# Kernel optimization log

Hardware: AMD Instinct MI355X
Metric: run time of the kernel (lower is better)

## Reference

```python
import jax, jax.numpy as jnp
import numpy as np

B = 32768          # number of trees
DEPTH = 3          # perfect binary trees: 8 leaves each
N_LEAF = B * (1 << DEPTH)
V, X, H, C = 32000, 256, 128, 5


def _apply_iou(iou, c, b_iou):
    # iou: [n, 3H], c: [n, H]
    i, o, u = jnp.split(iou + b_iou, 3, axis=1)
    c = jax.nn.sigmoid(i) * jnp.tanh(u) + c
    h = jax.nn.sigmoid(o) * jnp.tanh(c)
    return h, c


def setup_inputs() -> dict:
    key = jax.random.key(0)
    ks = jax.random.split(key, 8)
    rng = np.random.default_rng(0)

    # per-level random node orderings -> irregular child gathers
    sizes = [N_LEAF >> l for l in range(DEPTH + 1)]  # [8B, 4B, 2B, B]
    perms = [rng.permutation(s).astype(np.int32) for s in sizes]
    parts = []
    for l in range(1, DEPTH + 1):
        n = sizes[l]
        k = np.arange(n)
        ci = np.empty((n, 2), np.int32)
        # canonical node k at level l has children 2k, 2k+1 at level l-1
        ci[perms[l]] = np.stack([perms[l - 1][2 * k], perms[l - 1][2 * k + 1]], 1)
        parts.append(ci)
    child_idx = jnp.asarray(np.concatenate(parts, 0))  # [4B+2B+B, 2]

    leaf_x = jax.random.randint(ks[0], (N_LEAF,), 0, V, dtype=jnp.int32)
    sc = 0.02
    return {
        "leaf_x": leaf_x,
        "child_idx": child_idx,
        "emb": jax.random.normal(ks[1], (V, X), jnp.float32) * sc,
        "W_iou": jax.random.normal(ks[2], (3 * H, X), jnp.float32) * sc,
        "U_iou": jax.random.normal(ks[3], (3 * H, 2 * H), jnp.float32) * sc,
        "b_iou": jnp.zeros((3 * H,), jnp.float32),
        "U_f": jax.random.normal(ks[4], (2 * H, 2 * H), jnp.float32) * sc,
        "b_f": jnp.zeros((2 * H,), jnp.float32),
        "W_lin": jax.random.normal(ks[5], (C, H), jnp.float32) * sc,
        "b_lin": jnp.zeros((C,), jnp.float32),
    }


def reference(leaf_x, child_idx, emb, W_iou, U_iou, b_iou, U_f, b_f, W_lin, b_lin):
    # Leaves: embedding -> W_iou -> gates with c=0 (dropout is identity in eval)
    embeds = emb[leaf_x]                       # [N_leaf, X]
    iou = embeds @ W_iou.T                     # [N_leaf, 3H]
    h, c = _apply_iou(iou, jnp.zeros((leaf_x.shape[0], H), iou.dtype), b_iou)

    hs = [h]
    n, offset, total = leaf_x.shape[0], 0, child_idx.shape[0]
    while offset < total:  # one iteration per tree level (static)
        n //= 2
        ci = child_idx[offset:offset + n]       # [n, 2] -> prev-level rows
        offset += n
        h_ch = h[ci]                            # [n, 2, H] irregular gather
        c_ch = c[ci]                            # [n, 2, H]
        h_cat = h_ch.reshape(n, 2 * H)
        f = jax.nn.sigmoid(h_cat @ U_f.T + b_f).reshape(n, 2, H)
        c_sum = jnp.sum(f * c_ch, axis=1)       # [n, H]
        iou = h_cat @ U_iou.T                   # [n, 3H]
        h, c = _apply_iou(iou, c_sum, b_iou)
        hs.append(h)

    h_all = jnp.concatenate(hs, axis=0)         # [N_total, H]
    logits = h_all @ W_lin.T + b_lin            # [N_total, C]
    return logits
```

## Files before the change

### kernel.cpp

```cpp
#include <hip/hip_runtime.h>
#include <hip/hip_bf16.h>
#include <stdint.h>


#define THREADS 512

typedef __attribute__((ext_vector_type(8))) short short8;
typedef __attribute__((ext_vector_type(4))) float f32x4;

__device__ __forceinline__ unsigned short f2bf(float x) {
    unsigned u = __float_as_uint(x);
    u += 0x7fffu + ((u >> 16) & 1u);
    return (unsigned short)(u >> 16);
}
__device__ __forceinline__ float bf2f(unsigned short b) {
    return __uint_as_float(((unsigned)b) << 16);
}
__device__ __forceinline__ float rcp_fast(float x) { return __builtin_amdgcn_rcpf(x); }
__device__ __forceinline__ float sigm(float x) { return rcp_fast(1.f + __expf(-x)); }
__device__ __forceinline__ float tanh_fast(float x) {
    float e = __expf(2.f * x);
    return (e - 1.f) * rcp_fast(e + 1.f);
}

__global__ __launch_bounds__(256)
void prep_kernel(const float* __restrict__ W_iou,
                 const float* __restrict__ U_iou,
                 const float* __restrict__ U_f,
                 unsigned short* __restrict__ Wl,
                 unsigned short* __restrict__ Wc)
{
    const int i = blockIdx.x * 256 + threadIdx.x;
    if (i < 98304) {
        Wl[i] = f2bf(W_iou[i]);
        Wc[i] = f2bf(U_iou[i]);
    }
    if (i < 65536) {
        Wc[98304 + i] = f2bf(U_f[i]);
    }
}

template<int NCOL, int G, int CW, bool WC>
__device__ __forceinline__ void level_step(
    const unsigned short* __restrict__ Wg,
    const unsigned char* Blds,
    unsigned char* h_out,
    unsigned short* cAr,
    const float* __restrict__ b_iou, const float* __restrict__ b_f,
    int w, int lrow, int lk, int slotBase, int mrows)
{
    const int q0 = w * 16;
    const unsigned char* wbase = reinterpret_cast<const unsigned char*>(Wg)
                               + (q0 + lrow) * 512 + lk * 16;

    f32x4 acc[NCOL][G];
    #pragma unroll
    for (int j = 0; j < NCOL; ++j)
        #pragma unroll
        for (int g = 0; g < G; ++g)
            acc[j][g] = (f32x4){0.f, 0.f, 0.f, 0.f};

    #pragma unroll
    for (int ks = 0; ks < 8; ++ks) {
        short8 aW[NCOL];
        #pragma unroll
        for (int j = 0; j < NCOL; ++j)
            aW[j] = *reinterpret_cast<const short8*>(
                wbase + j * 65536 + ks * 64);
        #pragma unroll
        for (int g = 0; g < G; ++g) {
            const int row = g * 16 + lrow;
            const int chunk = (ks * 4 + lk) ^ (row & 7);
            short8 bN = *reinterpret_cast<const short8*>(
                Blds + row * 512 + (chunk << 4));
            #pragma unroll
            for (int j = 0; j < NCOL; ++j)
                acc[j][g] = __builtin_amdgcn_mfma_f32_16x16x32_bf16(
                    aW[j], bN, acc[j][g], 0, 0, 0);
        }
    }

    #pragma unroll
    for (int g = 0; g < G; ++g) {
        const int mlB = g * 16 + lrow;
        if (mlB < mrows) {
            const int ml = slotBase + mlB;
            #pragma unroll
            for (int r = 0; r < 4; ++r) {
                const int p = q0 + lk * 4 + r;
                float iv = acc[0][g][r] + b_iou[p];
                float ov = acc[1][g][r] + b_iou[128 + p];
                float uv = acc[2][g][r] + b_iou[256 + p];
                float csum = 0.f;
                if (NCOL == 5) {
                    float f0 = acc[3][g][r] + b_f[p];
                    float f1 = acc[4][g][r] + b_f[128 + p];
                    const int cb = p * 66 + CW * mlB;
                    csum = sigm(f0) * bf2f(cAr[cb])
                         + sigm(f1) * bf2f(cAr[cb + CW / 2]);
                }
                float cv = sigm(iv) * tanh_fast(uv) + csum;
                float hv = sigm(ov) * tanh_fast(cv);
                if (WC) cAr[p * 66 + CW * ml] = f2bf(cv);
                const int jr = ml >> 1;
                const int q = (ml & 1) * 16 + (p >> 3);
                *reinterpret_cast<unsigned short*>(
                    h_out + jr * 512 + ((q ^ (jr & 7)) << 4) + (p & 7) * 2)
                    = f2bf(hv);
            }
        }
    }
}

__device__ __forceinline__ void logits_emit(
    const unsigned char* h_lds, int M, const int* idsLds, int idBase,
    int segOff, const float* __restrict__ W_lin, const float* __restrict__ b_lin,
    float* __restrict__ out, int t)
{
    const int s = t >> 2, sub = t & 3;
    if (s >= M) return;
    float hv[32];
    const int j = s >> 1;
    #pragma unroll
    for (int qq = 0; qq < 4; ++qq) {
        const int q = (s & 1) * 16 + sub * 4 + qq;
        short8 v = *reinterpret_cast<const short8*>(
            h_lds + j * 512 + ((q ^ (j & 7)) << 4));
        #pragma unroll
        for (int e = 0; e < 8; ++e) hv[qq * 8 + e] = bf2f((unsigned short)v[e]);
    }
    const int gid = idsLds ? idsLds[s] : (idBase + s);
    float dots[5];
    #pragma unroll
    for (int cl = 0; cl < 5; ++cl) {
        const float* wr = W_lin + cl * 128 + sub * 32;
        float d = 0.f;
        #pragma unroll
        for (int k = 0; k < 32; ++k) d += hv[k] * wr[k];
        d += __shfl_xor(d, 1);
        d += __shfl_xor(d, 2);
        dots[cl] = d;
    }
    if (sub == 0) {
        float* op = out + (size_t)(segOff + gid) * 5;
        #pragma unroll
        for (int cl = 0; cl < 5; ++cl)
            op[cl] = dots[cl] + b_lin[cl];
    }
}

__global__ __launch_bounds__(THREADS, 4)
void tree_kernel(const int*  __restrict__ leaf_x,
                 const int2* __restrict__ cpairs,
                 const float* __restrict__ emb,
                 const unsigned short* __restrict__ Wl,
                 const unsigned short* __restrict__ Wc,
                 const float* __restrict__ b_iou,
                 const float* __restrict__ b_f,
                 const float* __restrict__ W_lin,
                 const float* __restrict__ b_lin,
                 float* __restrict__ out)
{
    __shared__ __align__(16) unsigned char arena[49664];
    __shared__ int ids0[64], ids1[32], ids2[16], tok[64];

    const int t    = threadIdx.x;
    const int lane = t & 63;
    const int w    = t >> 6;
    const int lrow = lane & 15;
    const int lk   = lane >> 4;
    const int blk3 = blockIdx.x * 8;

    if (t < 8)  { int2 p = cpairs[196608 + blk3 + t]; ids2[2*t] = p.x; ids2[2*t+1] = p.y; }
    __syncthreads();
    if (t < 16) { int2 p = cpairs[131072 + ids2[t]];  ids1[2*t] = p.x; ids1[2*t+1] = p.y; }
    __syncthreads();
    if (t < 32) { int2 p = cpairs[ids1[t]];           ids0[2*t] = p.x; ids0[2*t+1] = p.y; }
    __syncthreads();
    if (t < 64) { tok[t] = leaf_x[ids0[t]]; }
    __syncthreads();

    unsigned char*  X0  = arena;
    unsigned char*  h0  = arena + 16384;
    unsigned short* cAr = (unsigned short*)(arena + 32768);
    unsigned char*  h1  = arena;
    unsigned char*  h2  = arena + 16384;
    unsigned char*  h3  = arena + 8192;

    #pragma unroll 1
    for (int half = 0; half < 2; ++half) {
        {
            const int c  = t & 31;
            const int r0 = t >> 5;
            #pragma unroll
            for (int rr = 0; rr < 2; ++rr) {
                const int r  = r0 + rr * 16;
                const int gi = tok[half * 32 + r];
                const float4* src = reinterpret_cast<const float4*>(
                    emb + (size_t)gi * 256 + c * 8);
                float4 a = src[0], b = src[1];
                short8 v;
                v[0]=(short)f2bf(a.x); v[1]=(short)f2bf(a.y);
                v[2]=(short)f2bf(a.z); v[3]=(short)f2bf(a.w);
                v[4]=(short)f2bf(b.x); v[5]=(short)f2bf(b.y);
                v[6]=(short)f2bf(b.z); v[7]=(short)f2bf(b.w);
                *reinterpret_cast<short8*>(X0 + r * 512 + ((c ^ (r & 7)) << 4)) = v;
            }
        }
        __syncthreads();
        level_step<3, 2, 1, true>(Wl, X0, h0, cAr, b_iou, b_f,
                                  w, lrow, lk, half * 32, 32);
        __syncthreads();
    }

    logits_emit(h0, 64, ids0, 0, 0, W_lin, b_lin, out, t);
    level_step<5, 2, 2, true>(Wc, h0, h1, cAr, b_iou, b_f,
                              w, lrow, lk, 0, 32);
    __syncthreads();

    logits_emit(h1, 32, ids1, 0, 262144, W_lin, b_lin, out, t);
    level_step<5, 1, 4, true>(Wc, h1, h2, cAr, b_iou, b_f,
                              w, lrow, lk, 0, 16);
    __syncthreads();

    logits_emit(h2, 16, ids2, 0, 393216, W_lin, b_lin, out, t);
    level_step<5, 1, 8, false>(Wc, h2, h3, cAr, b_iou, b_f,
                               w, lrow, lk, 0, 8);
    __syncthreads();

    logits_emit(h3, 8, nullptr, blk3, 458752, W_lin, b_lin, out, t);
}

extern "C" void kernel_launch(void* const* d_in, const int* in_sizes, int n_in,
                              void* d_out, int out_size, void* d_ws, size_t ws_size,
                              hipStream_t stream)
{
    const int*   leaf_x = (const int*)d_in[0];
    const int*   child  = (const int*)d_in[1];
    const float* emb    = (const float*)d_in[2];
    const float* W_iou  = (const float*)d_in[3];
    const float* U_iou  = (const float*)d_in[4];
    const float* b_iou  = (const float*)d_in[5];
    const float* U_f    = (const float*)d_in[6];
    const float* b_f    = (const float*)d_in[7];
    const float* W_lin  = (const float*)d_in[8];
    const float* b_lin  = (const float*)d_in[9];
    float* out = (float*)d_out;

    char* ws = (char*)d_ws;
    unsigned short* Wl = (unsigned short*)ws;
    unsigned short* Wc = (unsigned short*)(ws + 196608);

    prep_kernel<<<384, 256, 0, stream>>>(W_iou, U_iou, U_f, Wl, Wc);

    tree_kernel<<<4096, THREADS, 0, stream>>>(
        leaf_x, (const int2*)child, emb, Wl, Wc,
        b_iou, b_f, W_lin, b_lin, out);
}
```

Baseline: 903.4 us.

## Stage logits densely per block and scatter in a separate kernel; cache biases in LDS

Instead of each block writing its 5-float logits directly to scattered output rows, the tree kernel now stores its 120 logit rows densely in workspace together with an index map, and a new scatter kernel writes them to their final positions and adds b_lin. The iou/f biases and W_lin are also copied into shared memory once per block, which removes repeated global loads in the gate epilogue and the logit dot products. The logit computation is restructured to accumulate straight from LDS weights. The cost is an extra kernel launch, an extra round trip of about 10 MB through workspace, and more LDS per block, which could lower occupancy.

```diff
diff --git a/kernel.cpp b/kernel.cpp
--- a/kernel.cpp
+++ b/kernel.cpp
@@ -46,7 +46,7 @@
     const unsigned char* Blds,
     unsigned char* h_out,
     unsigned short* cAr,
-    const float* __restrict__ b_iou, const float* __restrict__ b_f,
+    const float* bias,
     int w, int lrow, int lk, int slotBase, int mrows)
 {
     const int q0 = w * 16;
@@ -88,13 +88,13 @@
             #pragma unroll
             for (int r = 0; r < 4; ++r) {
                 const int p = q0 + lk * 4 + r;
-                float iv = acc[0][g][r] + b_iou[p];
-                float ov = acc[1][g][r] + b_iou[128 + p];
-                float uv = acc[2][g][r] + b_iou[256 + p];
+                float iv = acc[0][g][r] + bias[p];
+                float ov = acc[1][g][r] + bias[128 + p];
+                float uv = acc[2][g][r] + bias[256 + p];
                 float csum = 0.f;
                 if (NCOL == 5) {
-                    float f0 = acc[3][g][r] + b_f[p];
-                    float f1 = acc[4][g][r] + b_f[128 + p];
+                    float f0 = acc[3][g][r] + bias[384 + p];
+                    float f1 = acc[4][g][r] + bias[512 + p];
                     const int cb = p * 66 + CW * mlB;
                     csum = sigm(f0) * bf2f(cAr[cb])
                          + sigm(f1) * bf2f(cAr[cb + CW / 2]);
@@ -112,41 +112,49 @@
     }
 }
 
-__device__ __forceinline__ void logits_emit(
-    const unsigned char* h_lds, int M, const int* idsLds, int idBase,
-    int segOff, const float* __restrict__ W_lin, const float* __restrict__ b_lin,
-    float* __restrict__ out, int t)
+__device__ __forceinline__ void logits_stash(
+    const unsigned char* h_lds, int M, int stBase,
+    const float* Wl_lds, float* sL, int t)
 {
     const int s = t >> 2, sub = t & 3;
     if (s >= M) return;
-    float hv[32];
     const int j = s >> 1;
+    float dots[5] = {0.f, 0.f, 0.f, 0.f, 0.f};
     #pragma unroll
     for (int qq = 0; qq < 4; ++qq) {
         const int q = (s & 1) * 16 + sub * 4 + qq;
         short8 v = *reinterpret_cast<const short8*>(
             h_lds + j * 512 + ((q ^ (j & 7)) << 4));
         #pragma unroll
-        for (int e = 0; e < 8; ++e) hv[qq * 8 + e] = bf2f((unsigned short)v[e]);
-    }
-    const int gid = idsLds ? idsLds[s] : (idBase + s);
-    float dots[5];
+        for (int e = 0; e < 8; ++e) {
+            const float hv = bf2f((unsigned short)v[e]);
+            const int k = sub * 32 + qq * 8 + e;
+            #pragma unroll
+            for (int cl = 0; cl < 5; ++cl)
+                dots[cl] += hv * Wl_lds[cl * 128 + k];
+        }
+    }
     #pragma unroll
     for (int cl = 0; cl < 5; ++cl) {
-        const float* wr = W_lin + cl * 128 + sub * 32;
-        float d = 0.f;
-        #pragma unroll
-        for (int k = 0; k < 32; ++k) d += hv[k] * wr[k];
+        float d = dots[cl];
         d += __shfl_xor(d, 1);
         d += __shfl_xor(d, 2);
-        dots[cl] = d;
-    }
-    if (sub == 0) {
-        float* op = out + (size_t)(segOff + gid) * 5;
-        #pragma unroll
-        for (int cl = 0; cl < 5; ++cl)
-            op[cl] = dots[cl] + b_lin[cl];
-    }
+        if (sub == 0) sL[(stBase + s) * 5 + cl] = d;
+    }
+}
+
+__global__ __launch_bounds__(256)
+void scatter_kernel(const float* __restrict__ dense,
+                    const int* __restrict__ map,
+                    const float* __restrict__ b_lin,
+                    float* __restrict__ out)
+{
+    const int i = blockIdx.x * 256 + threadIdx.x;
+    const int g = map[i];
+    const float* sp = dense + (size_t)i * 5;
+    float* op = out + (size_t)g * 5;
+    #pragma unroll
+    for (int c = 0; c < 5; ++c) op[c] = sp[c] + b_lin[c];
 }
 
 __global__ __launch_bounds__(THREADS, 4)
@@ -158,11 +166,13 @@
                  const float* __restrict__ b_iou,
                  const float* __restrict__ b_f,
                  const float* __restrict__ W_lin,
-                 const float* __restrict__ b_lin,
-                 float* __restrict__ out)
+                 float* __restrict__ denseL,
+                 int* __restrict__ mapL)
 {
     __shared__ __align__(16) unsigned char arena[49664];
-    __shared__ int ids0[64], ids1[32], ids2[16], tok[64];
+    __shared__ int ids0[64], ids1[32], ids2[16], tok[64], sg[120];
+    __shared__ float sL[600];
+    __shared__ float bias[1280];
 
     const int t    = threadIdx.x;
     const int lane = t & 63;
@@ -171,13 +181,25 @@
     const int lk   = lane >> 4;
     const int blk3 = blockIdx.x * 8;
 
+    #pragma unroll
+    for (int i = t; i < 1280; i += THREADS) {
+        float v;
+        if (i < 384)      v = b_iou[i];
+        else if (i < 640) v = b_f[i - 384];
+        else              v = W_lin[i - 640];
+        bias[i] = v;
+    }
+
     if (t < 8)  { int2 p = cpairs[196608 + blk3 + t]; ids2[2*t] = p.x; ids2[2*t+1] = p.y; }
     __syncthreads();
     if (t < 16) { int2 p = cpairs[131072 + ids2[t]];  ids1[2*t] = p.x; ids1[2*t+1] = p.y; }
     __syncthreads();
     if (t < 32) { int2 p = cpairs[ids1[t]];           ids0[2*t] = p.x; ids0[2*t+1] = p.y; }
     __syncthreads();
-    if (t < 64) { tok[t] = leaf_x[ids0[t]]; }
+    if      (t < 64)  { tok[t] = leaf_x[ids0[t]]; sg[t] = ids0[t]; }
+    else if (t < 96)  { sg[t] = 262144 + ids1[t - 64]; }
+    else if (t < 112) { sg[t] = 393216 + ids2[t - 96]; }
+    else if (t < 120) { sg[t] = 458752 + blk3 + (t - 112); }
     __syncthreads();
 
     unsigned char*  X0  = arena;
@@ -186,6 +208,7 @@
     unsigned char*  h1  = arena;
     unsigned char*  h2  = arena + 16384;
     unsigned char*  h3  = arena + 8192;
+    const float*    WlL = bias + 640;
 
     #pragma unroll 1
     for (int half = 0; half < 2; ++half) {
@@ -208,27 +231,35 @@
             }
         }
         __syncthreads();
-        level_step<3, 2, 1, true>(Wl, X0, h0, cAr, b_iou, b_f,
+        level_step<3, 2, 1, true>(Wl, X0, h0, cAr, bias,
                                   w, lrow, lk, half * 32, 32);
         __syncthreads();
     }
 
-    logits_emit(h0, 64, ids0, 0, 0, W_lin, b_lin, out, t);
-    level_step<5, 2, 2, true>(Wc, h0, h1, cAr, b_iou, b_f,
+    logits_stash(h0, 64, 0, WlL, sL, t);
+    level_step<5, 2, 2, true>(Wc, h0, h1, cAr, bias,
                               w, lrow, lk, 0, 32);
     __syncthreads();
 
-    logits_emit(h1, 32, ids1, 0, 262144, W_lin, b_lin, out, t);
-    level_step<5, 1, 4, true>(Wc, h1, h2, cAr, b_iou, b_f,
+    logits_stash(h1, 32, 64, WlL, sL, t);
+    level_step<5, 1, 4, true>(Wc, h1, h2, cAr, bias,
                               w, lrow, lk, 0, 16);
     __syncthreads();
 
-    logits_emit(h2, 16, ids2, 0, 393216, W_lin, b_lin, out, t);
-    level_step<5, 1, 8, false>(Wc, h2, h3, cAr, b_iou, b_f,
+    logits_stash(h2, 16, 96, WlL, sL, t);
+    level_step<5, 1, 8, false>(Wc, h2, h3, cAr, bias,
                                w, lrow, lk, 0, 8);
     __syncthreads();
 
-    logits_emit(h3, 8, nullptr, blk3, 458752, W_lin, b_lin, out, t);
+    logits_stash(h3, 8, 112, WlL, sL, t);
+    __syncthreads();
+
+    {
+        float* dL = denseL + (size_t)blockIdx.x * 600;
+        int*   mp = mapL   + (size_t)blockIdx.x * 120;
+        if (t < 120) mp[t] = sg[t];
+        for (int i = t; i < 600; i += THREADS) dL[i] = sL[i];
+    }
 }
 
 extern "C" void kernel_launch(void* const* d_in, const int* in_sizes, int n_in,
@@ -250,10 +281,14 @@
     char* ws = (char*)d_ws;
     unsigned short* Wl = (unsigned short*)ws;
     unsigned short* Wc = (unsigned short*)(ws + 196608);
+    float* denseL = (float*)(ws + 524288);
+    int*   mapL   = (int*)(ws + 524288 + 9830400);
 
     prep_kernel<<<384, 256, 0, stream>>>(W_iou, U_iou, U_f, Wl, Wc);
 
     tree_kernel<<<4096, THREADS, 0, stream>>>(
         leaf_x, (const int2*)child, emb, Wl, Wc,
-        b_iou, b_f, W_lin, b_lin, out);
-}
+        b_iou, b_f, W_lin, denseL, mapL);
+
+    scatter_kernel<<<1920, 256, 0, stream>>>(denseL, mapL, b_lin, out);
+}
```

New measurement: 928.2 us. +2.7%, slower.

## Split tree kernel into per-level wave kernels with global h/c buffers

Applied to the files above, without the earlier changes.

Replaces the single block-per-8-trees kernel with a multi-launch pipeline. Child-index chasing kernels first build per-level node id lists. Then one wave-per-16-nodes MFMA kernel runs per level, storing h and c in workspace in bf16, with logits fused into the epilogue. This removes the LDS-heavy, sync-bound fused design and its low-occupancy 512-thread blocks, but adds global round trips for h/c, extra launches, and per-wave weight reloads from L2. The old fused kernel is kept as a fallback when the workspace is too small.

```diff
diff --git a/kernel.cpp b/kernel.cpp
--- a/kernel.cpp
+++ b/kernel.cpp
@@ -2,8 +2,6 @@
 #include <hip/hip_bf16.h>
 #include <stdint.h>
 
-
-#define THREADS 512
 
 typedef __attribute__((ext_vector_type(8))) short short8;
 typedef __attribute__((ext_vector_type(4))) float f32x4;
@@ -40,33 +38,174 @@
     }
 }
 
+__global__ __launch_bounds__(256)
+void chase_kernel(const int2* __restrict__ cp, const int* __restrict__ src,
+                  int srcBase, int n, int* __restrict__ dst)
+{
+    const int i = blockIdx.x * 256 + threadIdx.x;
+    if (i < n) {
+        const int s = src ? src[i] : srcBase + i;
+        const int2 c = cp[s];
+        dst[2 * i]     = c.x;
+        dst[2 * i + 1] = c.y;
+    }
+}
+
+template<int NCOL, bool LEAF, bool STORE_HC>
+__global__ __launch_bounds__(256)
+void wave_level(const unsigned short* __restrict__ Wg,
+                const int*  __restrict__ idlist,
+                int idbase,
+                const int*  __restrict__ leafx,
+                const float* __restrict__ emb,
+                const unsigned short* __restrict__ hprev,
+                const unsigned short* __restrict__ cprev,
+                unsigned short* __restrict__ hout,
+                unsigned short* __restrict__ cout,
+                const float* __restrict__ b_iou,
+                const float* __restrict__ b_f,
+                const float* __restrict__ W_lin,
+                const float* __restrict__ b_lin,
+                float* __restrict__ out, int segOff, int nnodes)
+{
+    const int lane = threadIdx.x & 63;
+    const int nb   = (blockIdx.x * 4 + (threadIdx.x >> 6)) * 16;
+    if (nb >= nnodes) return;
+    const int lrow = lane & 15;
+    const int lk   = lane >> 4;
+
+    short8 aN[8];
+    if (LEAF) {
+        const int li = idlist ? idlist[nb + lrow] : idbase + nb + lrow;
+        const int gi = leafx[li];
+        const float* er = emb + (size_t)gi * 256;
+        #pragma unroll
+        for (int ks = 0; ks < 8; ++ks) {
+            const float4 a = *reinterpret_cast<const float4*>(er + ks * 32 + lk * 8);
+            const float4 b = *reinterpret_cast<const float4*>(er + ks * 32 + lk * 8 + 4);
+            short8 v;
+            v[0]=(short)f2bf(a.x); v[1]=(short)f2bf(a.y);
+            v[2]=(short)f2bf(a.z); v[3]=(short)f2bf(a.w);
+            v[4]=(short)f2bf(b.x); v[5]=(short)f2bf(b.y);
+            v[6]=(short)f2bf(b.z); v[7]=(short)f2bf(b.w);
+            aN[ks] = v;
+        }
+    } else {
+        #pragma unroll
+        for (int ks = 0; ks < 8; ++ks) {
+            const int child = 2 * (nb + lrow) + (ks >= 4 ? 1 : 0);
+            aN[ks] = *reinterpret_cast<const short8*>(
+                hprev + (size_t)child * 128 + (ks & 3) * 32 + lk * 8);
+        }
+    }
+
+    int gidr[4];
+    #pragma unroll
+    for (int r = 0; r < 4; ++r) {
+        const int i = nb + lk * 4 + r;
+        gidr[r] = idlist ? idlist[i] : idbase + i;
+    }
+
+    float lgt[5][4];
+    #pragma unroll
+    for (int cl = 0; cl < 5; ++cl)
+        #pragma unroll
+        for (int r = 0; r < 4; ++r) lgt[cl][r] = 0.f;
+
+    for (int pb = 0; pb < 128; pb += 16) {
+        f32x4 acc[NCOL];
+        #pragma unroll
+        for (int j = 0; j < NCOL; ++j) acc[j] = (f32x4){0.f, 0.f, 0.f, 0.f};
+
+        #pragma unroll
+        for (int ks = 0; ks < 8; ++ks) {
+            short8 bW[NCOL];
+            #pragma unroll
+            for (int j = 0; j < NCOL; ++j)
+                bW[j] = *reinterpret_cast<const short8*>(
+                    Wg + (size_t)(j * 128 + pb + lrow) * 256 + ks * 32 + lk * 8);
+            #pragma unroll
+            for (int j = 0; j < NCOL; ++j)
+                acc[j] = __builtin_amdgcn_mfma_f32_16x16x32_bf16(
+                    aN[ks], bW[j], acc[j], 0, 0, 0);
+        }
+
+        const int p = pb + lrow;
+        const float bi = b_iou[p], bo = b_iou[128 + p], bu = b_iou[256 + p];
+        float bf0 = 0.f, bf1 = 0.f;
+        if (NCOL == 5) { bf0 = b_f[p]; bf1 = b_f[128 + p]; }
+        float wl[5];
+        #pragma unroll
+        for (int cl = 0; cl < 5; ++cl) wl[cl] = W_lin[cl * 128 + p];
+
+        #pragma unroll
+        for (int r = 0; r < 4; ++r) {
+            const int i = nb + lk * 4 + r;
+            const float iv = acc[0][r] + bi;
+            const float ov = acc[1][r] + bo;
+            const float uv = acc[2][r] + bu;
+            float csum = 0.f;
+            if (NCOL == 5) {
+                const float c0 = bf2f(cprev[(size_t)(2 * i) * 128 + p]);
+                const float c1 = bf2f(cprev[(size_t)(2 * i + 1) * 128 + p]);
+                csum = sigm(acc[3][r] + bf0) * c0 + sigm(acc[4][r] + bf1) * c1;
+            }
+            const float cv = sigm(iv) * tanh_fast(uv) + csum;
+            const float hv = sigm(ov) * tanh_fast(cv);
+            if (STORE_HC) {
+                hout[(size_t)i * 128 + p] = f2bf(hv);
+                cout[(size_t)i * 128 + p] = f2bf(cv);
+            }
+            #pragma unroll
+            for (int cl = 0; cl < 5; ++cl) lgt[cl][r] += hv * wl[cl];
+        }
+    }
+
+    #pragma unroll
+    for (int cl = 0; cl < 5; ++cl)
+        #pragma unroll
+        for (int r = 0; r < 4; ++r) {
+            float d = lgt[cl][r];
+            d += __shfl_xor(d, 1);
+            d += __shfl_xor(d, 2);
+            d += __shfl_xor(d, 4);
+            d += __shfl_xor(d, 8);
+            lgt[cl][r] = d;
+        }
+    if (lrow < 5) {
+        const float bl = b_lin[lrow];
+        #pragma unroll
+        for (int r = 0; r < 4; ++r) {
+            float v = (lrow == 0) ? lgt[0][r] : (lrow == 1) ? lgt[1][r]
+                    : (lrow == 2) ? lgt[2][r] : (lrow == 3) ? lgt[3][r] : lgt[4][r];
+            out[(size_t)(segOff + gidr[r]) * 5 + lrow] = v + bl;
+        }
+    }
+}
+
+#define FB_THREADS 512
+
 template<int NCOL, int G, int CW, bool WC>
-__device__ __forceinline__ void level_step(
+__device__ __forceinline__ void fb_level_step(
     const unsigned short* __restrict__ Wg,
-    const unsigned char* Blds,
-    unsigned char* h_out,
-    unsigned short* cAr,
+    const unsigned char* Blds, unsigned char* h_out, unsigned short* cAr,
     const float* __restrict__ b_iou, const float* __restrict__ b_f,
     int w, int lrow, int lk, int slotBase, int mrows)
 {
     const int q0 = w * 16;
     const unsigned char* wbase = reinterpret_cast<const unsigned char*>(Wg)
                                + (q0 + lrow) * 512 + lk * 16;
-
     f32x4 acc[NCOL][G];
     #pragma unroll
     for (int j = 0; j < NCOL; ++j)
         #pragma unroll
-        for (int g = 0; g < G; ++g)
-            acc[j][g] = (f32x4){0.f, 0.f, 0.f, 0.f};
-
+        for (int g = 0; g < G; ++g) acc[j][g] = (f32x4){0.f, 0.f, 0.f, 0.f};
     #pragma unroll
     for (int ks = 0; ks < 8; ++ks) {
         short8 aW[NCOL];
         #pragma unroll
         for (int j = 0; j < NCOL; ++j)
-            aW[j] = *reinterpret_cast<const short8*>(
-                wbase + j * 65536 + ks * 64);
+            aW[j] = *reinterpret_cast<const short8*>(wbase + j * 65536 + ks * 64);
         #pragma unroll
         for (int g = 0; g < G; ++g) {
             const int row = g * 16 + lrow;
@@ -79,7 +218,6 @@
                     aW[j], bN, acc[j][g], 0, 0, 0);
         }
     }
-
     #pragma unroll
     for (int g = 0; g < G; ++g) {
         const int mlB = g * 16 + lrow;
@@ -96,8 +234,7 @@
                     float f0 = acc[3][g][r] + b_f[p];
                     float f1 = acc[4][g][r] + b_f[128 + p];
                     const int cb = p * 66 + CW * mlB;
-                    csum = sigm(f0) * bf2f(cAr[cb])
-                         + sigm(f1) * bf2f(cAr[cb + CW / 2]);
+                    csum = sigm(f0) * bf2f(cAr[cb]) + sigm(f1) * bf2f(cAr[cb + CW / 2]);
                 }
                 float cv = sigm(iv) * tanh_fast(uv) + csum;
                 float hv = sigm(ov) * tanh_fast(cv);
@@ -105,14 +242,13 @@
                 const int jr = ml >> 1;
                 const int q = (ml & 1) * 16 + (p >> 3);
                 *reinterpret_cast<unsigned short*>(
-                    h_out + jr * 512 + ((q ^ (jr & 7)) << 4) + (p & 7) * 2)
-                    = f2bf(hv);
+                    h_out + jr * 512 + ((q ^ (jr & 7)) << 4) + (p & 7) * 2) = f2bf(hv);
             }
         }
     }
 }
 
-__device__ __forceinline__ void logits_emit(
+__device__ __forceinline__ void fb_logits_emit(
     const unsigned char* h_lds, int M, const int* idsLds, int idBase,
     int segOff, const float* __restrict__ W_lin, const float* __restrict__ b_lin,
     float* __restrict__ out, int t)
@@ -144,33 +280,27 @@
     if (sub == 0) {
         float* op = out + (size_t)(segOff + gid) * 5;
         #pragma unroll
-        for (int cl = 0; cl < 5; ++cl)
-            op[cl] = dots[cl] + b_lin[cl];
-    }
-}
-
-__global__ __launch_bounds__(THREADS, 4)
-void tree_kernel(const int*  __restrict__ leaf_x,
-                 const int2* __restrict__ cpairs,
-                 const float* __restrict__ emb,
-                 const unsigned short* __restrict__ Wl,
-                 const unsigned short* __restrict__ Wc,
-                 const float* __restrict__ b_iou,
-                 const float* __restrict__ b_f,
-                 const float* __restrict__ W_lin,
-                 const float* __restrict__ b_lin,
-                 float* __restrict__ out)
+        for (int cl = 0; cl < 5; ++cl) op[cl] = dots[cl] + b_lin[cl];
+    }
+}
+
+__global__ __launch_bounds__(FB_THREADS, 4)
+void fb_tree_kernel(const int*  __restrict__ leaf_x,
+                    const int2* __restrict__ cpairs,
+                    const float* __restrict__ emb,
+                    const unsigned short* __restrict__ Wl,
+                    const unsigned short* __restrict__ Wc,
+                    const float* __restrict__ b_iou,
+                    const float* __restrict__ b_f,
+                    const float* __restrict__ W_lin,
+                    const float* __restrict__ b_lin,
+                    float* __restrict__ out)
 {
     __shared__ __align__(16) unsigned char arena[49664];
     __shared__ int ids0[64], ids1[32], ids2[16], tok[64];
-
-    const int t    = threadIdx.x;
-    const int lane = t & 63;
-    const int w    = t >> 6;
-    const int lrow = lane & 15;
-    const int lk   = lane >> 4;
+    const int t = threadIdx.x, lane = t & 63, w = t >> 6;
+    const int lrow = lane & 15, lk = lane >> 4;
     const int blk3 = blockIdx.x * 8;
-
     if (t < 8)  { int2 p = cpairs[196608 + blk3 + t]; ids2[2*t] = p.x; ids2[2*t+1] = p.y; }
     __syncthreads();
     if (t < 16) { int2 p = cpairs[131072 + ids2[t]];  ids1[2*t] = p.x; ids1[2*t+1] = p.y; }
@@ -179,22 +309,19 @@
     __syncthreads();
     if (t < 64) { tok[t] = leaf_x[ids0[t]]; }
     __syncthreads();
-
     unsigned char*  X0  = arena;
     unsigned char*  h0  = arena + 16384;
     unsigned short* cAr = (unsigned short*)(arena + 32768);
     unsigned char*  h1  = arena;
     unsigned char*  h2  = arena + 16384;
     unsigned char*  h3  = arena + 8192;
-
     #pragma unroll 1
     for (int half = 0; half < 2; ++half) {
         {
-            const int c  = t & 31;
-            const int r0 = t >> 5;
+            const int c = t & 31, r0 = t >> 5;
             #pragma unroll
             for (int rr = 0; rr < 2; ++rr) {
-                const int r  = r0 + rr * 16;
+                const int r = r0 + rr * 16;
                 const int gi = tok[half * 32 + r];
                 const float4* src = reinterpret_cast<const float4*>(
                     emb + (size_t)gi * 256 + c * 8);
@@ -208,27 +335,20 @@
             }
         }
         __syncthreads();
-        level_step<3, 2, 1, true>(Wl, X0, h0, cAr, b_iou, b_f,
-                                  w, lrow, lk, half * 32, 32);
+        fb_level_step<3, 2, 1, true>(Wl, X0, h0, cAr, b_iou, b_f,
+                                     w, lrow, lk, half * 32, 32);
         __syncthreads();
     }
-
-    logits_emit(h0, 64, ids0, 0, 0, W_lin, b_lin, out, t);
-    level_step<5, 2, 2, true>(Wc, h0, h1, cAr, b_iou, b_f,
-                              w, lrow, lk, 0, 32);
-    __syncthreads();
-
-    logits_emit(h1, 32, ids1, 0, 262144, W_lin, b_lin, out, t);
-    level_step<5, 1, 4, true>(Wc, h1, h2, cAr, b_iou, b_f,
-                              w, lrow, lk, 0, 16);
-    __syncthreads();
-
-    logits_emit(h2, 16, ids2, 0, 393216, W_lin, b_lin, out, t);
-    level_step<5, 1, 8, false>(Wc, h2, h3, cAr, b_iou, b_f,
-                               w, lrow, lk, 0, 8);
-    __syncthreads();
-
-    logits_emit(h3, 8, nullptr, blk3, 458752, W_lin, b_lin, out, t);
+    fb_logits_emit(h0, 64, ids0, 0, 0, W_lin, b_lin, out, t);
+    fb_level_step<5, 2, 2, true>(Wc, h0, h1, cAr, b_iou, b_f, w, lrow, lk, 0, 32);
+    __syncthreads();
+    fb_logits_emit(h1, 32, ids1, 0, 262144, W_lin, b_lin, out, t);
+    fb_level_step<5, 1, 4, true>(Wc, h1, h2, cAr, b_iou, b_f, w, lrow, lk, 0, 16);
+    __syncthreads();
+    fb_logits_emit(h2, 16, ids2, 0, 393216, W_lin, b_lin, out, t);
+    fb_level_step<5, 1, 8, false>(Wc, h2, h3, cAr, b_iou, b_f, w, lrow, lk, 0, 8);
+    __syncthreads();
+    fb_logits_emit(h3, 8, nullptr, blk3, 458752, W_lin, b_lin, out, t);
 }
 
 extern "C" void kernel_launch(void* const* d_in, const int* in_sizes, int n_in,
@@ -251,9 +371,59 @@
     unsigned short* Wl = (unsigned short*)ws;
     unsigned short* Wc = (unsigned short*)(ws + 196608);
 
+    auto need = [](int s) -> size_t {
+        const size_t n3 = 32768u / s, n2 = 2 * n3, n1 = 2 * n2, n0 = 2 * n1;
+        size_t off = 524288;
+        off += (n0 + n1 + n2) * 4;
+        off = (off + 255) & ~(size_t)255;
+        off += (n0 + n0 + n1 + n1) * 256;
+        return off;
+    };
+    int s = 0;
+    if      (ws_size >= need(1)) s = 1;
+    else if (ws_size >= need(2)) s = 2;
+    else if (ws_size >= need(4)) s = 4;
+
     prep_kernel<<<384, 256, 0, stream>>>(W_iou, U_iou, U_f, Wl, Wc);
 
-    tree_kernel<<<4096, THREADS, 0, stream>>>(
-        leaf_x, (const int2*)child, emb, Wl, Wc,
-        b_iou, b_f, W_lin, b_lin, out);
-}
+    if (s == 0) {
+        fb_tree_kernel<<<4096, FB_THREADS, 0, stream>>>(
+            leaf_x, (const int2*)child, emb, Wl, Wc,
+            b_iou, b_f, W_lin, b_lin, out);
+        return;
+    }
+
+    const int n3 = 32768 / s, n2 = 2 * n3, n1 = 2 * n2, n0 = 2 * n1;
+    size_t off = 524288;
+    int* ids0 = (int*)(ws + off); off += (size_t)n0 * 4;
+    int* ids1 = (int*)(ws + off); off += (size_t)n1 * 4;
+    int* ids2 = (int*)(ws + off); off += (size_t)n2 * 4;
+    off = (off + 255) & ~(size_t)255;
+    unsigned short* h0 = (unsigned short*)(ws + off); off += (size_t)n0 * 256;
+    unsigned short* c0 = (unsigned short*)(ws + off); off += (size_t)n0 * 256;
+    unsigned short* h1 = (unsigned short*)(ws + off); off += (size_t)n1 * 256;
+    unsigned short* c1 = (unsigned short*)(ws + off);
+    unsigned short* h2 = h0;
+    unsigned short* c2 = c0;
+
+    const int2* cp = (const int2*)child;
+    for (int sp = 0; sp < s; ++sp) {
+        const int r3 = sp * n3;
+        chase_kernel<<<(n3 + 255) / 256, 256, 0, stream>>>(cp + 196608, nullptr, r3, n3, ids2);
+        chase_kernel<<<(n2 + 255) / 256, 256, 0, stream>>>(cp + 131072, ids2, 0, n2, ids1);
+        chase_kernel<<<(n1 + 255) / 256, 256, 0, stream>>>(cp,          ids1, 0, n1, ids0);
+
+        wave_level<3, true, true><<<n0 / 64, 256, 0, stream>>>(
+            Wl, ids0, 0, leaf_x, emb, nullptr, nullptr, h0, c0,
+            b_iou, b_f, W_lin, b_lin, out, 0, n0);
+        wave_level<5, false, true><<<n1 / 64, 256, 0, stream>>>(
+            Wc, ids1, 0, nullptr, nullptr, h0, c0, h1, c1,
+            b_iou, b_f, W_lin, b_lin, out, 262144, n1);
+        wave_level<5, false, true><<<n2 / 64, 256, 0, stream>>>(
+            Wc, ids2, 0, nullptr, nullptr, h1, c1, h2, c2,
+            b_iou, b_f, W_lin, b_lin, out, 393216, n2);
+        wave_level<5, false, false><<<n3 / 64, 256, 0, stream>>>(
+            Wc, nullptr, r3, nullptr, nullptr, h2, c2, nullptr, nullptr,
+            b_iou, b_f, W_lin, b_lin, out, 458752, n3);
+    }
+}
```

New measurement: 987.6 us. 1.09x slower.
